# Kernel tuning notes

Measured on AMD Instinct MI355X. Metric: run time of the kernel, lower is better.

Reference implementation:

```python
import jax, jax.numpy as jnp
import numpy as np

B, C, H, W = 32, 3, 512, 512
EPS = 1e-8


def _radius_bins(h, w):
    cy, cx = h // 2, w // 2
    y = jnp.arange(h, dtype=jnp.float32) - cy
    x = jnp.arange(w, dtype=jnp.float32) - cx
    radius = jnp.sqrt(y[:, None] ** 2 + x[None, :] ** 2)  # [H, W]
    max_r = min(cy, cx)
    bins = jnp.floor(radius).astype(jnp.int32)
    # pixels with radius >= max_r fall outside all bins in the original loop;
    # route them to a dummy overflow bin that we drop afterwards.
    bins = jnp.where(bins < max_r, bins, max_r)
    return bins.reshape(-1), max_r


def _psd(x):
    f = jnp.fft.fft2(x)                  # over last two dims, like torch.fft.fft2
    psd = jnp.abs(f) ** 2
    return jnp.log(psd + EPS)            # log_power=True


def _radial_average(psd):
    b, c, h, w = psd.shape
    bins, max_r = _radius_bins(h, w)     # [H*W], static
    data = psd.reshape(b * c, h * w).T   # [H*W, B*C]
    sums = jax.ops.segment_sum(data, bins, num_segments=max_r + 1)
    counts = jax.ops.segment_sum(jnp.ones((h * w,), psd.dtype), bins,
                                 num_segments=max_r + 1)
    avg = jnp.where(counts[:, None] > 0, sums / counts[:, None], 0.0)
    avg = avg[:max_r]                    # drop overflow bin -> [max_r, B*C]
    return avg.T.reshape(b, c, max_r)


def setup_inputs() -> dict:
    key = jax.random.key(0)
    k1, k2 = jax.random.split(key)
    predicted = jax.random.normal(k1, (B, C, H, W), dtype=jnp.float32)
    target = jax.random.normal(k2, (B, C, H, W), dtype=jnp.float32)
    return {"predicted": predicted, "target": target}


def reference(predicted, target):
    pred_rad = _radial_average(_psd(predicted))
    targ_rad = _radial_average(_psd(target))
    return jnp.mean(jnp.abs(pred_rad - targ_rad))  # l1, reduction='mean'
```

## Files before the change

### kernel.cpp

```cpp
#include <hip/hip_runtime.h>
#include <math.h>

#define HH 512
#define WW 512
#define IMG (HH*WW)
#define NIMG_PER 96
#define NIMG 192
#define NBIN 256
#define EPSV 1e-8f

#define CSTR 264
#define IMGC (512*CSTR)
#define SLOT 580

__device__ __forceinline__ int drev(int s) {
    return ((s & 7) << 6) | (s & 56) | (s >> 6);
}
__device__ __forceinline__ int fsw(int a) { return a + (a >> 3); }

__device__ __forceinline__ float2 cmul(float2 a, float2 b) {
    return make_float2(a.x*b.x - a.y*b.y, a.x*b.y + a.y*b.x);
}
#define C_ADD(a,b) make_float2((a).x+(b).x, (a).y+(b).y)
#define C_SUB(a,b) make_float2((a).x-(b).x, (a).y-(b).y)
#define C_NI(a)    make_float2((a).y, -(a).x)

__device__ __forceinline__ void bfly8(float2 x[8]) {
    const float R = 0.70710678118654752440f;
    float2 t0=C_ADD(x[0],x[4]), t4=C_SUB(x[0],x[4]);
    float2 t1=C_ADD(x[1],x[5]), t5=C_SUB(x[1],x[5]);
    float2 t2=C_ADD(x[2],x[6]), t6=C_SUB(x[2],x[6]);
    float2 t3=C_ADD(x[3],x[7]), t7=C_SUB(x[3],x[7]);
    float2 u0=C_ADD(t0,t2), u2=C_SUB(t0,t2);
    float2 u1=C_ADD(t1,t3), u3=C_SUB(t1,t3);
    x[0]=C_ADD(u0,u1); x[4]=C_SUB(u0,u1);
    { float2 n3 = C_NI(u3); x[2]=C_ADD(u2,n3); x[6]=C_SUB(u2,n3); }
    float2 s1 = make_float2(R*(t5.x + t5.y), R*(t5.y - t5.x));
    float2 s2 = C_NI(t6);
    float2 s3 = make_float2(R*(t7.y - t7.x), -R*(t7.x + t7.y));
    float2 v0=C_ADD(t4,s2), v2=C_SUB(t4,s2);
    float2 v1=C_ADD(s1,s3), v3=C_SUB(s1,s3);
    x[1]=C_ADD(v0,v1); x[5]=C_SUB(v0,v1);
    { float2 n3 = C_NI(v3); x[3]=C_ADD(v2,n3); x[7]=C_SUB(v2,n3); }
}

__device__ __forceinline__ void twiddle7(float2* x, float ang) {
    const float sn = __sinf(ang), cs = __cosf(ang);
    const float2 w1 = make_float2(cs, sn);
    const float2 w2 = cmul(w1, w1);
    const float2 w3 = cmul(w2, w1);
    const float2 w4 = cmul(w2, w2);
    const float2 w5 = cmul(w2, w3);
    const float2 w6 = cmul(w3, w3);
    const float2 w7 = cmul(w3, w4);
    x[1]=cmul(x[1],w1); x[2]=cmul(x[2],w2); x[3]=cmul(x[3],w3);
    x[4]=cmul(x[4],w4); x[5]=cmul(x[5],w5); x[6]=cmul(x[6],w6);
    x[7]=cmul(x[7],w7);
}

__global__ __launch_bounds__(256) void rowfft_kernel(
    const float* __restrict__ pred, const float* __restrict__ targ,
    float2* __restrict__ out, int img_base)
{
    __shared__ float2 sd[2320];
    const int t = threadIdx.x;

    const int pb = blockIdx.x;
    const int li = blockIdx.y;
    const int g  = img_base + li;
    const float* img = (g < NIMG_PER) ? (pred + (size_t)g * IMG)
                                      : (targ + (size_t)(g - NIMG_PER) * IMG);
    const float4* src4 = (const float4*)(img + (size_t)(pb*8) * WW);

    #pragma unroll
    for (int it = 0; it < 2; ++it) {
        const int id = it*256 + t;
        const int s  = id >> 7;
        const int x4 = id & 127;
        const float4 va = src4[(2*s)   * 128 + x4];
        const float4 vb = src4[(2*s+1) * 128 + x4];
        float2* p = sd + s*SLOT + (4*x4 + (x4 >> 1));
        p[0] = make_float2(va.x, vb.x);
        p[1] = make_float2(va.y, vb.y);
        p[2] = make_float2(va.z, vb.z);
        p[3] = make_float2(va.w, vb.w);
    }
    __syncthreads();

    const int i = t & 63;
    float2* p = sd + (t >> 6) * SLOT;
    float2 x[8];

    #pragma unroll
    for (int j = 0; j < 8; ++j) x[j] = p[fsw(i + 64*j)];
    bfly8(x);
    twiddle7(x, -0.012271846303085130f * (float)i);
    #pragma unroll
    for (int j = 0; j < 8; ++j) p[fsw(i + 64*j)] = x[j];
    __syncthreads();

    const int grp = i >> 3, i2 = i & 7;
    #pragma unroll
    for (int j = 0; j < 8; ++j) x[j] = p[fsw(64*grp + i2 + 8*j)];
    bfly8(x);
    twiddle7(x, -0.098174770424681038f * (float)i2);
    #pragma unroll
    for (int j = 0; j < 8; ++j) p[fsw(64*grp + i2 + 8*j)] = x[j];
    __syncthreads();

    #pragma unroll
    for (int j = 0; j < 8; ++j) x[j] = p[fsw(8*i + j)];
    bfly8(x);
    #pragma unroll
    for (int j = 0; j < 8; ++j) p[fsw(8*i + j)] = x[j];
    __syncthreads();

    const int w_ = t >> 6;
    const int k  = (w_ > 0) ? (((t & 7) << 6) | (t & 56) | w_)
                            : ((t < 32) ? (8*t + 4) : (8*(t - 32)));
    const int kk = (k <= 256) ? k : (512 - k);
    const int a1 = fsw(drev(kk));
    const int a2 = fsw(drev((512 - kk) & 511));
    const int a3 = fsw(drev(256));

    float2 A[4], Bv[4], Z[4];
    #pragma unroll
    for (int s = 0; s < 4; ++s) {
        const float2 P = sd[s*SLOT + a1];
        const float2 Q = sd[s*SLOT + a2];
        A[s]  = make_float2(0.5f*(P.x + Q.x), 0.5f*(P.y - Q.y));
        Bv[s] = make_float2(0.5f*(P.y + Q.y), 0.5f*(Q.x - P.x));
        Z[s]  = sd[s*SLOT + a3];
    }
    __syncthreads();

    {
        const int fb = fsw(kk);
        #pragma unroll
        for (int s = 0; s < 4; ++s) {
            sd[(2*s+0)*290 + fb] = A[s];
            sd[(2*s+1)*290 + fb] = Bv[s];
        }
    }
    if (t == 0) {
        const int fb = fsw(256);
        #pragma unroll
        for (int s = 0; s < 4; ++s) {
            sd[(2*s+0)*290 + fb] = make_float2(Z[s].x, 0.0f);
            sd[(2*s+1)*290 + fb] = make_float2(Z[s].y, 0.0f);
        }
    }
    __syncthreads();

    float2* dst = out + (size_t)li * IMGC + (size_t)(pb*8) * CSTR;
    #pragma unroll
    for (int r = 0; r < 8; ++r) {
        dst[(size_t)r * CSTR + t] = sd[r*290 + fsw(t)];
        if (t < 8) {
            float2 v = make_float2(0.0f, 0.0f);
            if (t == 0) v = sd[r*290 + fsw(256)];
            dst[(size_t)r * CSTR + 256 + t] = v;
        }
    }
}

__global__ __launch_bounds__(256) void colfft_kernel(
    const float2* __restrict__ in, float* __restrict__ bins, int img_base)
{
    __shared__ float2 sd[8*SLOT];
    __shared__ float  bs[4*257];
    const int t = threadIdx.x;
    #pragma unroll
    for (int id = t; id < 4*257; id += 256) bs[id] = 0.0f;

    const int li = blockIdx.y;
    const int x0 = blockIdx.x * 8;
    const float2* src = in + (size_t)li * IMGC;

    #pragma unroll
    for (int it = 0; it < 16; ++it) {
        const int id = it*256 + t;
        const int y  = id >> 3;
        const int cl = id & 7;
        sd[cl*SLOT + fsw(y)] = src[(size_t)y * CSTR + (x0 + cl)];
    }
    __syncthreads();

    const int i  = t & 63;
    const int c0 = t >> 6;
    float2 x[2][8];

    #pragma unroll
    for (int sl = 0; sl < 2; ++sl) {
        float2* p = sd + (c0 + 4*sl)*SLOT;
        #pragma unroll
        for (int j = 0; j < 8; ++j) x[sl][j] = p[fsw(i + 64*j)];
        bfly8(x[sl]);
    }
    {
        const float ang = -0.012271846303085130f * (float)i;
        const float sn = __sinf(ang), cs = __cosf(ang);
        const float2 w1 = make_float2(cs, sn);
        const float2 w2 = cmul(w1,w1), w3 = cmul(w2,w1), w4 = cmul(w2,w2);
        const float2 w5 = cmul(w2,w3), w6 = cmul(w3,w3), w7 = cmul(w3,w4);
        #pragma unroll
        for (int sl = 0; sl < 2; ++sl) {
            x[sl][1]=cmul(x[sl][1],w1); x[sl][2]=cmul(x[sl][2],w2);
            x[sl][3]=cmul(x[sl][3],w3); x[sl][4]=cmul(x[sl][4],w4);
            x[sl][5]=cmul(x[sl][5],w5); x[sl][6]=cmul(x[sl][6],w6);
            x[sl][7]=cmul(x[sl][7],w7);
        }
    }
    #pragma unroll
    for (int sl = 0; sl < 2; ++sl) {
        float2* p = sd + (c0 + 4*sl)*SLOT;
        #pragma unroll
        for (int j = 0; j < 8; ++j) p[fsw(i + 64*j)] = x[sl][j];
    }
    __syncthreads();

    const int grp = i >> 3, i2 = i & 7;
    #pragma unroll
    for (int sl = 0; sl < 2; ++sl) {
        float2* p = sd + (c0 + 4*sl)*SLOT;
        #pragma unroll
        for (int j = 0; j < 8; ++j) x[sl][j] = p[fsw(64*grp + i2 + 8*j)];
        bfly8(x[sl]);
    }
    {
        const float ang = -0.098174770424681038f * (float)i2;
        const float sn = __sinf(ang), cs = __cosf(ang);
        const float2 w1 = make_float2(cs, sn);
        const float2 w2 = cmul(w1,w1), w3 = cmul(w2,w1), w4 = cmul(w2,w2);
        const float2 w5 = cmul(w2,w3), w6 = cmul(w3,w3), w7 = cmul(w3,w4);
        #pragma unroll
        for (int sl = 0; sl < 2; ++sl) {
            x[sl][1]=cmul(x[sl][1],w1); x[sl][2]=cmul(x[sl][2],w2);
            x[sl][3]=cmul(x[sl][3],w3); x[sl][4]=cmul(x[sl][4],w4);
            x[sl][5]=cmul(x[sl][5],w5); x[sl][6]=cmul(x[sl][6],w6);
            x[sl][7]=cmul(x[sl][7],w7);
        }
    }
    #pragma unroll
    for (int sl = 0; sl < 2; ++sl) {
        float2* p = sd + (c0 + 4*sl)*SLOT;
        #pragma unroll
        for (int j = 0; j < 8; ++j) p[fsw(64*grp + i2 + 8*j)] = x[sl][j];
    }
    __syncthreads();

    const int rep = ((i >> 3) & 3) * 257;
    #pragma unroll
    for (int sl = 0; sl < 2; ++sl) {
        const int cl = c0 + 4*sl;
        const int kx = x0 + cl;
        float2* p = sd + cl*SLOT;
        float2 y8[8];
        #pragma unroll
        for (int j = 0; j < 8; ++j) y8[j] = p[fsw(8*i + j)];
        bfly8(y8);
        if (kx <= 256) {
            const float wgt = (kx == 0 || kx == 256) ? 1.0f : 2.0f;
            const int dx = kx - 256;
            const int cbase = 8*(i & 7) + (i >> 3);
            #pragma unroll
            for (int j = 0; j < 8; ++j) {
                const int ky = 64*j + cbase;
                const float val = __logf(y8[j].x*y8[j].x + y8[j].y*y8[j].y + EPSV);
                const int dy = ky - 256;
                const int b  = (int)sqrtf((float)(dy*dy + dx*dx));
                if (b < NBIN) atomicAdd(&bs[rep + b], wgt * val);
            }
        }
    }
    __syncthreads();

    const float v = bs[t] + bs[257 + t] + bs[514 + t] + bs[771 + t];
    atomicAdd(&bins[(size_t)(img_base + li) * NBIN + t], v);
}

__global__ __launch_bounds__(256) void counts_kernel(float* __restrict__ cnt)
{
    __shared__ float c[NBIN];
    const int t = threadIdx.x;
    c[t] = 0.0f;
    __syncthreads();

    const int base = blockIdx.x * 4096;
    #pragma unroll
    for (int i = 0; i < 16; ++i) {
        const int id = base + i * 256 + t;
        const int y = id >> 9, xx = id & 511;
        const int dy = y - 256, dx = xx - 256;
        const int b  = (int)sqrtf((float)(dy*dy + dx*dx));
        if (b < NBIN) atomicAdd(&c[b], 1.0f);
    }
    __syncthreads();
    if (c[t] != 0.0f) atomicAdd(&cnt[t], c[t]);
}

__global__ __launch_bounds__(256) void finalize_kernel(
    const float* __restrict__ bins, const float* __restrict__ cnt,
    float* __restrict__ out)
{
    __shared__ float red[256];
    const int t = threadIdx.x;

    float acc = 0.0f;
    for (int id = t; id < NIMG_PER * NBIN; id += 256) {
        const int i = id >> 8;
        const int r = id & 255;
        const float d = fabsf(bins[(size_t)i * NBIN + r]
                            - bins[(size_t)(NIMG_PER + i) * NBIN + r]);
        acc += d / cnt[r];
    }
    red[t] = acc;
    __syncthreads();
    for (int w = 128; w > 0; w >>= 1) {
        if (t < w) red[t] += red[t + w];
        __syncthreads();
    }
    if (t == 0) out[0] = red[0] / (float)(NIMG_PER * NBIN);
}

extern "C" void kernel_launch(void* const* d_in, const int* in_sizes, int n_in,
                              void* d_out, int out_size, void* d_ws, size_t ws_size,
                              hipStream_t stream)
{
    const float* pred = (const float*)d_in[0];
    const float* targ = (const float*)d_in[1];
    float* out = (float*)d_out;

    char* ws = (char*)d_ws;
    float* bins = (float*)ws;
    float* cnt  = bins + (size_t)NIMG * NBIN;
    const size_t zero_bytes = ((size_t)NIMG * NBIN + NBIN) * sizeof(float);
    const size_t off = (zero_bytes + 255) & ~(size_t)255;
    float2* cbuf = (float2*)(ws + off);

    const size_t per_img = (size_t)IMGC * sizeof(float2);
    size_t avail = (ws_size > off) ? (ws_size - off) : 0;
    int chunk = (int)(avail / per_img);
    if (chunk > NIMG) chunk = NIMG;
    if (chunk < 1) chunk = 1;

    hipMemsetAsync(bins, 0, zero_bytes, stream);
    counts_kernel<<<dim3(64), dim3(256), 0, stream>>>(cnt);

    for (int base = 0; base < NIMG; base += chunk) {
        const int n = (NIMG - base < chunk) ? (NIMG - base) : chunk;
        dim3 gA(HH / 8, n), gB(33, n), blk(256);
        rowfft_kernel<<<gA, blk, 0, stream>>>(pred, targ, cbuf, base);
        colfft_kernel<<<gB, blk, 0, stream>>>(cbuf, bins, base);
    }

    finalize_kernel<<<dim3(1), dim3(256), 0, stream>>>(bins, cnt, out);
}
```

Baseline: 259.4 us.

## Run-length merge radial bins and replace global atomics with partial-sum reduction

The column-FFT epilogue now writes its butterfly outputs back to shared memory. Each thread then walks 16 consecutive ky values in one column and merges runs that land in the same radius bin before doing a shared atomic, so far fewer LDS atomics are issued. The per-tile global atomicAdd into the bins is replaced by a plain store into a per-tile partial buffer. A new reduce kernel sums the 33 partials per image, which removes the memset of the bins array. The cost is an extra shared-memory round trip, an extra kernel launch, and a larger workspace that leaves less room for the FFT chunk buffer.

New measurement: 238.7 us. 1.09x faster.

```diff
diff --git a/kernel.cpp b/kernel.cpp
--- a/kernel.cpp
+++ b/kernel.cpp
@@ -11,6 +11,7 @@
 
 #define CSTR 264
 #define IMGC (512*CSTR)
+#define NTILE 33
 #define SLOT 580
 
 __device__ __forceinline__ int drev(int s) {
@@ -165,12 +166,11 @@
 }
 
 __global__ __launch_bounds__(256) void colfft_kernel(
-    const float2* __restrict__ in, float* __restrict__ bins, int img_base)
+    const float2* __restrict__ in, float* __restrict__ bins2, int img_base)
 {
     __shared__ float2 sd[8*SLOT];
     __shared__ float  bs[4*257];
     const int t = threadIdx.x;
-    #pragma unroll
     for (int id = t; id < 4*257; id += 256) bs[id] = 0.0f;
 
     const int li = blockIdx.y;
@@ -249,34 +249,61 @@
     }
     __syncthreads();
 
-    const int rep = ((i >> 3) & 3) * 257;
-    #pragma unroll
-    for (int sl = 0; sl < 2; ++sl) {
-        const int cl = c0 + 4*sl;
-        const int kx = x0 + cl;
-        float2* p = sd + cl*SLOT;
+    #pragma unroll
+    for (int sl = 0; sl < 2; ++sl) {
+        float2* p = sd + (c0 + 4*sl)*SLOT;
         float2 y8[8];
         #pragma unroll
         for (int j = 0; j < 8; ++j) y8[j] = p[fsw(8*i + j)];
         bfly8(y8);
-        if (kx <= 256) {
-            const float wgt = (kx == 0 || kx == 256) ? 1.0f : 2.0f;
-            const int dx = kx - 256;
-            const int cbase = 8*(i & 7) + (i >> 3);
-            #pragma unroll
-            for (int j = 0; j < 8; ++j) {
-                const int ky = 64*j + cbase;
-                const float val = __logf(y8[j].x*y8[j].x + y8[j].y*y8[j].y + EPSV);
-                const int dy = ky - 256;
-                const int b  = (int)sqrtf((float)(dy*dy + dx*dx));
-                if (b < NBIN) atomicAdd(&bs[rep + b], wgt * val);
+        #pragma unroll
+        for (int j = 0; j < 8; ++j) p[fsw(8*i + j)] = y8[j];
+    }
+    __syncthreads();
+
+    {
+        const int cl2 = t & 7;
+        const int h   = t >> 3;
+        const int kx  = x0 + cl2;
+        const bool valid = (kx <= 256);
+        const float scale = (kx == 0 || kx == 256) ? 0.5f : 1.0f;
+        const int dxsq = (kx - 256) * (kx - 256);
+        const int rep  = (t & 3) * 257;
+
+        float acc = 0.0f;
+        int prevb = 1000;
+        #pragma unroll
+        for (int j = 0; j < 16; ++j) {
+            const int q = 64*(j & 7) + 8*((2*h + (j >> 3)) & 7) + (h >> 2);
+            const float2 v = sd[cl2*SLOT + fsw(q)];
+            const float val = __logf(v.x*v.x + v.y*v.y + EPSV) * scale;
+            const int dy = 16*h + j - 256;
+            const int b  = (int)sqrtf((float)(dy*dy + dxsq));
+            if (b != prevb) {
+                if (prevb < NBIN && valid) atomicAdd(&bs[rep + prevb], acc);
+                prevb = b; acc = val;
+            } else {
+                acc += val;
             }
         }
-    }
-    __syncthreads();
-
-    const float v = bs[t] + bs[257 + t] + bs[514 + t] + bs[771 + t];
-    atomicAdd(&bins[(size_t)(img_base + li) * NBIN + t], v);
+        if (prevb < NBIN && valid) atomicAdd(&bs[rep + prevb], acc);
+    }
+    __syncthreads();
+
+    const float v = 2.0f * (bs[t] + bs[257 + t] + bs[514 + t] + bs[771 + t]);
+    bins2[((size_t)blockIdx.x * NIMG + (img_base + li)) * NBIN + t] = v;
+}
+
+__global__ __launch_bounds__(256) void reduce_kernel(
+    const float* __restrict__ bins2, float* __restrict__ bins)
+{
+    const int li = blockIdx.x;
+    const int t  = threadIdx.x;
+    float s = 0.0f;
+    #pragma unroll
+    for (int tile = 0; tile < NTILE; ++tile)
+        s += bins2[((size_t)tile * NIMG + li) * NBIN + t];
+    bins[(size_t)li * NBIN + t] = s;
 }
 
 __global__ __launch_bounds__(256) void counts_kernel(float* __restrict__ cnt)
@@ -332,10 +359,11 @@
     float* out = (float*)d_out;
 
     char* ws = (char*)d_ws;
-    float* bins = (float*)ws;
-    float* cnt  = bins + (size_t)NIMG * NBIN;
-    const size_t zero_bytes = ((size_t)NIMG * NBIN + NBIN) * sizeof(float);
-    const size_t off = (zero_bytes + 255) & ~(size_t)255;
+    float* cnt   = (float*)ws;
+    float* bins  = cnt + NBIN;
+    float* bins2 = bins + (size_t)NIMG * NBIN;
+    const size_t fixed_f = NBIN + (size_t)NIMG*NBIN + (size_t)NTILE*NIMG*NBIN;
+    const size_t off = (fixed_f*sizeof(float) + 255) & ~(size_t)255;
     float2* cbuf = (float2*)(ws + off);
 
     const size_t per_img = (size_t)IMGC * sizeof(float2);
@@ -344,15 +372,16 @@
     if (chunk > NIMG) chunk = NIMG;
     if (chunk < 1) chunk = 1;
 
-    hipMemsetAsync(bins, 0, zero_bytes, stream);
+    hipMemsetAsync(cnt, 0, NBIN * sizeof(float), stream);
     counts_kernel<<<dim3(64), dim3(256), 0, stream>>>(cnt);
 
     for (int base = 0; base < NIMG; base += chunk) {
         const int n = (NIMG - base < chunk) ? (NIMG - base) : chunk;
-        dim3 gA(HH / 8, n), gB(33, n), blk(256);
+        dim3 gA(HH / 8, n), gB(NTILE, n), blk(256);
         rowfft_kernel<<<gA, blk, 0, stream>>>(pred, targ, cbuf, base);
-        colfft_kernel<<<gB, blk, 0, stream>>>(cbuf, bins, base);
-    }
-
+        colfft_kernel<<<gB, blk, 0, stream>>>(cbuf, bins2, base);
+    }
+
+    reduce_kernel<<<dim3(NIMG), dim3(256), 0, stream>>>(bins2, bins);
     finalize_kernel<<<dim3(1), dim3(256), 0, stream>>>(bins, cnt, out);
 }
```
